# Performance work log

Measured on AMD Instinct MI355X. Metric: run time of the kernel, lower is better.

The kernel has to match this reference:

```python
import jax, jax.numpy as jnp
import numpy as np

NE, NT, NC, D, NR = 100000, 1024, 128, 128, 500
H, E, L_GCN = 8, 4, 2
B, DEG = 512, 8
NSRC = B * DEG
NNZ_E2T, NNZ_T2C, NNZ_E2C = 1000000, 50000, 500000
TAU, DECAY, CLW = 0.5, 1e-4, 0.1
N_NODES = NE + NT + NC


def setup_inputs() -> dict:
    ks = iter(jax.random.split(jax.random.key(0), 64))
    def n(shape, s=0.05):
        return jax.random.normal(next(ks), shape, jnp.float32) * s
    def ri(shape, hi):
        return jax.random.randint(next(ks), shape, 0, hi, jnp.int32)
    def u(shape):
        return jax.random.uniform(next(ks), shape, jnp.float32) * 0.01
    T = NT
    return {
        'entity_emb': n((NE, D)), 'type_emb': n((NT, D)), 'cluster_emb': n((NC, D)),
        'relation': n((NR, 2 * D)),
        'ln_g': jnp.ones((D,), jnp.float32), 'ln_b': jnp.zeros((D,), jnp.float32),
        'cl_w1': n((D, D)), 'cl_b1': jnp.zeros((D,), jnp.float32),
        'cl_w2': n((D, D)), 'cl_b2': jnp.zeros((D,), jnp.float32),
        'fc_w': n((2 * D, T)), 'fc_b': jnp.zeros((T,), jnp.float32),
        'wq': n((T, T)), 'bq': jnp.zeros((T,), jnp.float32),
        'wk': n((T, T)), 'bk': jnp.zeros((T,), jnp.float32),
        'wv': n((T, T)), 'bv': jnp.zeros((T,), jnp.float32),
        'wo': n((T, T)), 'bo': jnp.zeros((T,), jnp.float32),
        'gate_w': n((T, E)), 'exp_w': n((E, T, T)), 'exp_b': jnp.zeros((E, T), jnp.float32),
        'e2t_val': u((NNZ_E2T,)), 't2c_val': u((NNZ_T2C,)), 'e2c_val': u((NNZ_E2C,)),
        'e2t_row': ri((NNZ_E2T,), NE + NT), 'e2t_col': ri((NNZ_E2T,), NE + NT),
        't2c_row': ri((NNZ_T2C,), NT + NC), 't2c_col': ri((NNZ_T2C,), NT + NC),
        'e2c_row': ri((NNZ_E2C,), NE + NC), 'e2c_col': ri((NNZ_E2C,), NE + NC),
        'src_ids': ri((NSRC,), N_NODES), 'etype': ri((NSRC,), 2 * NR),
    }


def _light_gcn(ea, eb, row, col, val, na, nb):
    x = jnp.concatenate([ea, eb], axis=0)
    acc = x
    for _ in range(L_GCN):  # fixed small layer count
        x = jax.ops.segment_sum(val[:, None] * x[col], row, num_segments=na + nb)
        acc = acc + x
    m = acc / (L_GCN + 1)
    return m[:na], m[na:]


def _ln(x, g, b):
    mu = x.mean(-1, keepdims=True)
    var = x.var(-1, keepdims=True)
    return (x - mu) * jax.lax.rsqrt(var + 1e-5) * g + b


def _cl_loss(src1, src2, w1, b1, w2, b2):
    def proj(x):
        return jax.nn.elu(x @ w1 + b1) @ w2 + b2
    def norm(x):
        return x / jnp.maximum(jnp.linalg.norm(x, axis=1, keepdims=True), 1e-12)
    z1, z2 = norm(proj(src1)), norm(proj(src2))
    s11 = jnp.exp(z1 @ z1.T / TAU)   # [N,N]
    s12 = jnp.exp(z1 @ z2.T / TAU)
    s22 = jnp.exp(z2 @ z2.T / TAU)
    d12 = jnp.diag(s12)
    l1 = -jnp.log(d12 / (s11.sum(1) + s12.sum(1) - jnp.diag(s11)))
    l2 = -jnp.log(d12 / (s22.sum(1) + s12.sum(0) - jnp.diag(s22)))
    return ((l1 + l2) * 0.5).mean()


def _mha_moe(x, wq, bq, wk, bk, wv, bv, wo, bo, gate_w, exp_w, exp_b):
    # x: [B, DEG, T]; MHA over mailbox axis, then softmax-gated MoE, mean-pool.
    b, l, t = x.shape
    dh = t // H
    q = (x @ wq + bq).reshape(b, l, H, dh)
    k = (x @ wk + bk).reshape(b, l, H, dh)
    v = (x @ wv + bv).reshape(b, l, H, dh)
    attn = jax.nn.softmax(jnp.einsum('blhd,bmhd->bhlm', q, k) / jnp.sqrt(jnp.float32(dh)), axis=-1)
    o = jnp.einsum('bhlm,bmhd->blhd', attn, v).reshape(b, l, t) @ wo + bo
    gate = jax.nn.softmax(o @ gate_w, axis=-1)               # [B,L,E]
    eo = jnp.einsum('blt,etu->bleu', o, exp_w) + exp_b       # [B,L,E,T]
    moe = jnp.einsum('ble,blet->blt', gate, eo)
    return moe.mean(axis=1)                                  # [B,T]


def reference(entity_emb, type_emb, cluster_emb, relation, ln_g, ln_b,
              cl_w1, cl_b1, cl_w2, cl_b2, fc_w, fc_b,
              wq, bq, wk, bk, wv, bv, wo, bo, gate_w, exp_w, exp_b,
              e2t_val, t2c_val, e2c_val,
              e2t_row, e2t_col, t2c_row, t2c_col, e2c_row, e2c_col,
              src_ids, etype):
    e2t_e, e2t_t = _light_gcn(entity_emb, type_emb, e2t_row, e2t_col, e2t_val, NE, NT)
    t2c_t, t2c_c = _light_gcn(type_emb, cluster_emb, t2c_row, t2c_col, t2c_val, NT, NC)
    e2c_e, e2c_c = _light_gcn(entity_emb, cluster_emb, e2c_row, e2c_col, e2c_val, NE, NC)
    # with_norm=True path; dropout is eval-mode identity
    e2t_e, e2t_t = _ln(e2t_e, ln_g, ln_b), _ln(e2t_t, ln_g, ln_b)
    t2c_t, t2c_c = _ln(t2c_t, ln_g, ln_b), _ln(t2c_c, ln_g, ln_b)
    e2c_e, e2c_c = _ln(e2c_e, ln_g, ln_b), _ln(e2c_c, ln_g, ln_b)
    node1 = jnp.concatenate([e2t_e, e2t_t, t2c_c], axis=0)
    node2 = jnp.concatenate([e2c_e, t2c_t, e2c_c], axis=0)
    src1 = node1[src_ids]   # [NSRC, D]
    src2 = node2[src_ids]
    cl = _cl_loss(src1, src2, cl_w1, cl_b1, cl_w2, cl_b2)
    src = jnp.concatenate([src1, src2], axis=-1)  # [NSRC, 2D]
    sign = jnp.where(etype >= NR, -1.0, 1.0).astype(jnp.float32)[:, None]
    rel = relation[etype % NR] * sign
    emb_loss = DECAY * ((src ** 2).sum() + (rel ** 2).sum()) * 0.5 / rel.shape[0]
    aux_loss = CLW * cl + emb_loss
    # update_all: u_add_e message, regular mailbox [B, DEG, 2D]
    msg = jax.nn.relu(src + rel).reshape(B, DEG, 2 * D)
    predict = msg @ fc_w + fc_b                                  # [B, DEG, NT]
    predict = _mha_moe(predict, wq, bq, wk, bk, wv, bv, wo, bo, gate_w, exp_w, exp_b)
    out = jax.nn.sigmoid(predict)                                # [B, NT]
    return out, aux_loss
```

## Files before the change

kernel.cpp:

```cpp
#include <hip/hip_runtime.h>
#include <hip/hip_bf16.h>
#include <cmath>

constexpr int cNE = 100000, cNT = 1024, cNC = 128, cD = 128, cNR = 500;
constexpr int cB = 512, cNSRC = 4096, cT = 1024, cE = 4;
constexpr int cNNZ_E2T = 1000000, cNNZ_T2C = 50000, cNNZ_E2C = 500000;
constexpr float cDECAY = 1e-4f, cCLW = 0.1f;
constexpr int cNN_E2T = cNE + cNT;
constexpr int cNN_E2C = cNE + cNC;
constexpr int cNN_T2C = cNT + cNC;

constexpr size_t F_S1   = 0;
constexpr size_t F_S2   = F_S1 + 524288;
constexpr size_t F_PT   = F_S2 + 524288;
constexpr size_t F_Z1   = F_PT + 524288;
constexpr size_t F_Z2   = F_Z1 + 524288;
constexpr size_t F_MSG  = F_Z2 + 524288;
constexpr size_t F_GATE = F_MSG + 524288;
constexpr size_t F_SCAL = F_GATE + 16384;
constexpr size_t F_RS   = F_SCAL + 64;
constexpr size_t F_D11  = F_RS + 16384;
constexpr size_t F_D12  = F_D11 + 4096;
constexpr size_t F_D22  = F_D12 + 4096;
constexpr size_t F_U    = F_D22 + 4096;
constexpr size_t G_X1F  = F_U;
constexpr size_t G_X2C  = G_X1F + 6465536;
constexpr size_t G_SLOT = G_X2C + 262144;
constexpr size_t G_REP  = G_SLOT + 101376;
constexpr size_t G_RP   = G_REP + 4096;
constexpr size_t G_FILL = G_RP + 101376;
constexpr size_t G_COLS = G_FILL + 101376;
constexpr size_t G_VALS = G_COLS + 1000000;
constexpr size_t G_X1T  = G_VALS + 1000000;
constexpr size_t G_X2T  = G_X1T + 73728;
constexpr size_t G_BSUM = G_X2T + 73728;
constexpr size_t A_U0  = F_U;
constexpr size_t A_U1  = F_U + 2097152;
constexpr size_t A_WBT = F_U + 4 * 2097152;

typedef __attribute__((ext_vector_type(8))) short short8v;
typedef __attribute__((ext_vector_type(4))) float f32x4;

__device__ __forceinline__ void atomAdd(float* p, float v) {
  __hip_atomic_fetch_add(p, v, __ATOMIC_RELAXED, __HIP_MEMORY_SCOPE_AGENT);
}
__device__ __forceinline__ ushort f2bf(float f) {
  __hip_bfloat16 h = __float2bfloat16(f);
  return *reinterpret_cast<ushort*>(&h);
}
__device__ __forceinline__ float bf2f(ushort u) {
  __hip_bfloat16 h; *reinterpret_cast<ushort*>(&h) = u;
  return __bfloat162float(h);
}

__device__ __forceinline__ int mapNode(int mode, int id) {
  switch (mode) {
    case 0:  return (id < cNE + cNT) ? id : -1;
    case 1:  return (id >= cNE + cNT) ? (id - cNE) : -1;
    case 2:  return (id >= cNE && id < cNE + cNT) ? (id - cNE) : -1;
    default: return (id < cNE) ? id
                   : ((id >= cNE + cNT) ? (id - cNT) : -1);
  }
}

__device__ __forceinline__ float blockReduce256(float v, float* sh, int tid) {
  sh[tid] = v; __syncthreads();
  for (int s = 128; s > 0; s >>= 1) {
    if (tid < s) sh[tid] += sh[tid + s];
    __syncthreads();
  }
  float r = sh[0]; __syncthreads();
  return r;
}

__global__ __launch_bounds__(256) void k_init3(int* __restrict__ slot, int* __restrict__ mark,
                                               int* __restrict__ fill, int n) {
  int i = blockIdx.x * 256 + threadIdx.x;
  if (i < n) { slot[i] = 0x7f7f7f7f; mark[i] = 0; fill[i] = 0; }
}

__global__ __launch_bounds__(256) void k_slot_mark(const int* __restrict__ ids,
                                                   int* __restrict__ slot,
                                                   int* __restrict__ mark, int mode) {
  int i = blockIdx.x * 256 + threadIdx.x;
  if (i >= cNSRC) return;
  int node = mapNode(mode, ids[i]);
  if (node >= 0) { atomicMin(&slot[node], i); mark[node] = 1; }
}

__global__ __launch_bounds__(256) void k_mark_edges(const int* __restrict__ row,
                                                    const int* __restrict__ col, int nnz,
                                                    const int* __restrict__ slot,
                                                    int* __restrict__ mark) {
  int e = blockIdx.x * 256 + threadIdx.x;
  if (e >= nnz) return;
  int r = row[e];
  if (slot[r] < cNSRC) mark[col[e]] = 1;
}

__global__ __launch_bounds__(256) void k_hist(const int* __restrict__ row, int nnz,
                                              const int* __restrict__ mark,
                                              int* __restrict__ cnt) {
  int e = blockIdx.x * 256 + threadIdx.x;
  if (e >= nnz) return;
  int r = row[e];
// ... 32 lines not shown
  }
  if (tid < nb) bsum[tid] = sh[tid] - v;
  if (tid == 511) rowptr[n] = sh[511];
}

__global__ __launch_bounds__(256) void k_scan_add(int* __restrict__ rowptr,
                                                  const int* __restrict__ bsum, int n,
                                                  int* __restrict__ fill) {
  int i = blockIdx.x * 256 + threadIdx.x;
  if (i < n) {
    int r = rowptr[i] + bsum[blockIdx.x];
    rowptr[i] = r;
    fill[i] = r;
  }
}

__global__ __launch_bounds__(256) void k_fill(const int* __restrict__ row,
                                              const int* __restrict__ col,
                                              const float* __restrict__ val, int nnz,
                                              const int* __restrict__ mark,
                                              int* __restrict__ fill,
                                              int* __restrict__ cols, float* __restrict__ vals) {
  int e = blockIdx.x * 256 + threadIdx.x;
  if (e >= nnz) return;
  int r = row[e];
  if (mark && !mark[r]) return;
  int pos = atomicAdd(&fill[r], 1);
  cols[pos] = col[e];
  vals[pos] = val[e];
}

__global__ __launch_bounds__(256) void k_gather(
    const int* __restrict__ rowptr, const int* __restrict__ cols, const float* __restrict__ vals,
    const float* __restrict__ ea, const float* __restrict__ eb, int na,
    int nrows, const int* __restrict__ mark, ushort* __restrict__ out) {
  int r = blockIdx.x * 4 + (threadIdx.x >> 6);
  if (r >= nrows) return;
  if (mark && !mark[r]) return;
  int lane = threadIdx.x & 63;
  int p0 = rowptr[r], p1 = rowptr[r + 1];
  float ax = 0.f, ay = 0.f;
  int p = p0;
  for (; p + 2 <= p1; p += 2) {
    int c0 = cols[p], c1 = cols[p + 1];
    float v0 = vals[p], v1 = vals[p + 1];
    const float* s0 = (c0 < na) ? (ea + (size_t)c0 * cD) : (eb + (size_t)(c0 - na) * cD);
    const float* s1 = (c1 < na) ? (ea + (size_t)c1 * cD) : (eb + (size_t)(c1 - na) * cD);
    float2 x0 = *reinterpret_cast<const float2*>(s0 + lane * 2);
    float2 x1 = *reinterpret_cast<const float2*>(s1 + lane * 2);
    ax += v0 * x0.x + v1 * x1.x;
    ay += v0 * x0.y + v1 * x1.y;
  }
  if (p < p1) {
    int c = cols[p];
    float v = vals[p];
    const float* s = (c < na) ? (ea + (size_t)c * cD) : (eb + (size_t)(c - na) * cD);
    float2 x = *reinterpret_cast<const float2*>(s + lane * 2);
    ax += v * x.x; ay += v * x.y;
  }
  ushort2 o; o.x = f2bf(ax); o.y = f2bf(ay);
  *reinterpret_cast<ushort2*>(out + (size_t)r * cD + lane * 2) = o;
}

__global__ __launch_bounds__(256) void k_rep(const int* __restrict__ ids,
                                             const int* __restrict__ slot, int mode,
                                             int* __restrict__ rep) {
  int i = blockIdx.x * 256 + threadIdx.x;
  if (i >= cNSRC) return;
  int node = mapNode(mode, ids[i]);
  rep[i] = (node >= 0 && slot[node] == i) ? node : -1;
}

__global__ __launch_bounds__(256) void k_gather_slot(
    const int* __restrict__ rowptr, const int* __restrict__ cols, const float* __restrict__ vals,
    const ushort* __restrict__ x1, const int* __restrict__ rep,
    ushort* __restrict__ outc) {
  int i = blockIdx.x * 4 + (threadIdx.x >> 6);
  if (i >= cNSRC) return;
  int r = rep[i];
  if (r < 0) return;
  int lane = threadIdx.x & 63;
  int p0 = rowptr[r], p1 = rowptr[r + 1];
  float ax = 0.f, ay = 0.f;
  int p = p0;
  for (; p + 2 <= p1; p += 2) {
    int c0 = cols[p], c1 = cols[p + 1];
    float v0 = vals[p], v1 = vals[p + 1];
    ushort2 x0 = *reinterpret_cast<const ushort2*>(x1 + (size_t)c0 * cD + lane * 2);
    ushort2 x1v = *reinterpret_cast<const ushort2*>(x1 + (size_t)c1 * cD + lane * 2);
    ax += v0 * bf2f(x0.x) + v1 * bf2f(x1v.x);
    ay += v0 * bf2f(x0.y) + v1 * bf2f(x1v.y);
  }
  if (p < p1) {
    int c = cols[p];
    float v = vals[p];
    ushort2 x = *reinterpret_cast<const ushort2*>(x1 + (size_t)c * cD + lane * 2);
    ax += v * bf2f(x.x); ay += v * bf2f(x.y);
  }
  ushort2 o; o.x = f2bf(ax); o.y = f2bf(ay);
  *reinterpret_cast<ushort2*>(outc + (size_t)i * cD + lane * 2) = o;
}

__global__ __launch_bounds__(256) void k_gather_bf(
    const int* __restrict__ rowptr, const int* __restrict__ cols, const float* __restrict__ vals,
    const ushort* __restrict__ x1, int nrows, ushort* __restrict__ out) {
  int r = blockIdx.x * 4 + (threadIdx.x >> 6);
  if (r >= nrows) return;
  int lane = threadIdx.x & 63;
  int p0 = rowptr[r], p1 = rowptr[r + 1];
  float ax = 0.f, ay = 0.f;
  for (int p = p0; p < p1; ++p) {
    int c = cols[p];
    float v = vals[p];
    ushort2 x = *reinterpret_cast<const ushort2*>(x1 + (size_t)c * cD + lane * 2);
    ax += v * bf2f(x.x); ay += v * bf2f(x.y);
  }
  ushort2 o; o.x = f2bf(ax); o.y = f2bf(ay);
  *reinterpret_cast<ushort2*>(out + (size_t)r * cD + lane * 2) = o;
}

__global__ __launch_bounds__(128) void gather_ln(
    const int* __restrict__ ids, int mode,
    const float* __restrict__ ea, const float* __restrict__ eb, int na,
    const ushort* __restrict__ x1, const ushort* __restrict__ x2, const int* __restrict__ slot,
    const float* __restrict__ g, const float* __restrict__ bia, float* __restrict__ dst) {
  __shared__ float shx[2], shy[2];
// ... 178 lines not shown
      short8v af[2], bfr[2];
#pragma unroll
      for (int i = 0; i < 2; ++i)
        af[i] = *reinterpret_cast<const short8v*>(&As[(wr + i * 16 + la) * 40 + lk]);
#pragma unroll
      for (int j = 0; j < 2; ++j)
        bfr[j] = *reinterpret_cast<const short8v*>(&Bs[(wc + j * 16 + la) * 40 + lk]);
#pragma unroll
      for (int i = 0; i < 2; ++i)
#pragma unroll
        for (int j = 0; j < 2; ++j)
          acc[i][j] = __builtin_amdgcn_mfma_f32_16x16x32_bf16(af[i], bfr[j], acc[i][j], 0, 0, 0);
    }
  }
  const int r0 = by * 64 + wr + (lane >> 4) * 4;
  const int c0 = bx * 64 + wc + la;
#pragma unroll
  for (int i = 0; i < 2; ++i)
#pragma unroll
    for (int q = 0; q < 4; ++q) {
      int r = r0 + i * 16 + q;
      float4 gv = *reinterpret_cast<const float4*>(gsum + r * 4);
#pragma unroll
      for (int j = 0; j < 2; ++j) {
        int c = c0 + j * 16;
        float bias = gv.x * expb[c] + gv.y * expb[1024 + c] +
                     gv.z * expb[2048 + c] + gv.w * expb[3072 + c];
        float s = (acc[i][j][q] + bias) * 0.125f;
        out[(size_t)r * 1024 + c] = 1.0f / (1.0f + expf(-s));
      }
    }
}

__global__ __launch_bounds__(256) void gram_sym(
    const ushort* __restrict__ W, float* __restrict__ rsum,
    float* __restrict__ d11, float* __restrict__ d12, float* __restrict__ d22) {
  __shared__ ushort As[128 * 40];
  __shared__ ushort Bs[128 * 40];
  int tt = blockIdx.x, bi = 0, cnt = 64;
  while (tt >= cnt) { tt -= cnt; ++bi; --cnt; }
  int bj = bi + tt;
  const bool diag = (bi == bj);
  const int t = threadIdx.x;
  const int wv = t >> 6, lane = t & 63;
  const int wr = (wv >> 1) * 64, wc = (wv & 1) * 64;
  const int srow = t >> 1, shalf = t & 1;
  const ushort* Ag = W + (size_t)(bi * 128 + srow) * 128 + shalf * 16;
  const ushort* Bg = W + (size_t)(bj * 128 + srow) * 128 + shalf * 16;
  uint4 ra0 = *reinterpret_cast<const uint4*>(Ag);
  uint4 ra1 = *reinterpret_cast<const uint4*>(Ag + 8);
  uint4 rb0 = *reinterpret_cast<const uint4*>(Bg);
  uint4 rb1 = *reinterpret_cast<const uint4*>(Bg + 8);
  f32x4 acc[4][4];
  const f32x4 z4 = {0.f, 0.f, 0.f, 0.f};
#pragma unroll
  for (int i = 0; i < 4; ++i)
#pragma unroll
    for (int j = 0; j < 4; ++j) acc[i][j] = z4;
  const int la = lane & 15, lk = (lane >> 4) * 8;
  const int sdst = srow * 40 + shalf * 16;
  for (int kt = 0; kt < 128; kt += 32) {
    __syncthreads();
    *reinterpret_cast<uint4*>(&As[sdst])     = ra0;
    *reinterpret_cast<uint4*>(&As[sdst + 8]) = ra1;
    *reinterpret_cast<uint4*>(&Bs[sdst])     = rb0;
    *reinterpret_cast<uint4*>(&Bs[sdst + 8]) = rb1;
    __syncthreads();
    if (kt + 32 < 128) {
      ra0 = *reinterpret_cast<const uint4*>(Ag + kt + 32);
      ra1 = *reinterpret_cast<const uint4*>(Ag + kt + 40);
      rb0 = *reinterpret_cast<const uint4*>(Bg + kt + 32);
      rb1 = *reinterpret_cast<const uint4*>(Bg + kt + 40);
    }
    short8v af[4], bfr[4];
#pragma unroll
    for (int i = 0; i < 4; ++i)
      af[i] = *reinterpret_cast<const short8v*>(&As[(wr + i * 16 + la) * 40 + lk]);
#pragma unroll
    for (int j = 0; j < 4; ++j)
      bfr[j] = *reinterpret_cast<const short8v*>(&Bs[(wc + j * 16 + la) * 40 + lk]);
#pragma unroll
    for (int i = 0; i < 4; ++i)
#pragma unroll
      for (int j = 0; j < 4; ++j)
        acc[i][j] = __builtin_amdgcn_mfma_f32_16x16x32_bf16(af[i], bfr[j], acc[i][j], 0, 0, 0);
  }
  const int r0 = bi * 128 + wr + (lane >> 4) * 4;
  const int c0 = bj * 128 + wc + la;
  constexpr float K2 = 2.8853900817779268f;
  float rs[4][4];
  float cs[4] = {0.f, 0.f, 0.f, 0.f};
#pragma unroll
  for (int i = 0; i < 4; ++i)
#pragma unroll
    for (int q = 0; q < 4; ++q) rs[i][q] = 0.f;
#pragma unroll
  for (int i = 0; i < 4; ++i)
#pragma unroll
    for (int j = 0; j < 4; ++j)
#pragma unroll
      for (int q = 0; q < 4; ++q) {
        int r = r0 + i * 16 + q;
        int c = c0 + j * 16;
        float e = exp2f(K2 * acc[i][j][q]);
        rs[i][q] += e;
        cs[j] += e;
        if (c == r)        { if (r < 4096) d11[r] = e; else d22[r - 4096] = e; }
        if (c == r + 4096) d12[r] = e;
      }
#pragma unroll
  for (int m = 1; m < 16; m <<= 1)
#pragma unroll
    for (int i = 0; i < 4; ++i)
#pragma unroll
      for (int q = 0; q < 4; ++q) rs[i][q] += __shfl_xor(rs[i][q], m);
  float* rowdst = rsum + ((bj >= 32) ? 8192 : 0);
  if (la == 0) {
#pragma unroll
    for (int i = 0; i < 4; ++i)
#pragma unroll
      for (int q = 0; q < 4; ++q) atomAdd(&rowdst[r0 + i * 16 + q], rs[i][q]);
  }
  if (!diag) {
#pragma unroll
    for (int j = 0; j < 4; ++j) {
      cs[j] += __shfl_xor(cs[j], 16);
      cs[j] += __shfl_xor(cs[j], 32);
    }
    float* coldst = rsum + ((bi >= 32) ? 8192 : 0);
    if ((lane >> 4) == 0) {
#pragma unroll
      for (int j = 0; j < 4; ++j) atomAdd(&coldst[c0 + j * 16], cs[j]);
    }
  }
}

__global__ __launch_bounds__(256) void cl_row(
    const float* __restrict__ rsum, const float* __restrict__ d11,
    const float* __restrict__ d12, const float* __restrict__ d22,
    float* __restrict__ cl_sum) {
  __shared__ float sh[256];
  int i = blockIdx.x * 256 + threadIdx.x;
  float denA = rsum[i] + rsum[8192 + i] - d11[i];
  float denB = rsum[8192 + 4096 + i] + rsum[4096 + i] - d22[i];
  float l = 0.5f * (logf(denA) + logf(denB)) - logf(d12[i]);
  float s = blockReduce256(l, sh, threadIdx.x);
  if (threadIdx.x == 0) atomAdd(cl_sum, s);
}

__global__ __launch_bounds__(256) void k_wt_bt(const float* __restrict__ W,
                                               ushort* __restrict__ Bt, int K, int N) {
  __shared__ float tile[32][33];
  int n0 = blockIdx.x * 32, k0 = blockIdx.y * 32;
  int tx = threadIdx.x & 31, ty = threadIdx.x >> 5;
#pragma unroll
  for (int i = 0; i < 4; ++i)
    tile[ty + 8 * i][tx] = W[(size_t)(k0 + ty + 8 * i) * N + n0 + tx];
  __syncthreads();
#pragma unroll
  for (int i = 0; i < 4; ++i)
    Bt[(size_t)(n0 + ty + 8 * i) * K + k0 + tx] = f2bf(tile[tx][ty + 8 * i]);
}

__global__ __launch_bounds__(256) void k_wt_bt_s(const float* __restrict__ Wbase,
                                                 ushort* __restrict__ Btbase, int K, int N) {
// ... 152 lines not shown
  const int* t2c_row = (const int*)d_in[28];
  const int* t2c_col = (const int*)d_in[29];
  const int* e2c_row = (const int*)d_in[30];
  const int* e2c_col = (const int*)d_in[31];
  const int* src_ids = (const int*)d_in[32];
  const int* etype   = (const int*)d_in[33];

  float* ws = (float*)d_ws;
  float* S1 = ws + F_S1;
  float* S2 = ws + F_S2;
  ushort* Wbf = (ushort*)(ws + F_PT);
  ushort* P1bf = (ushort*)(ws + F_Z1);
  ushort* SBbf = (ushort*)(ws + F_Z2);
  ushort* MSGbf = (ushort*)(ws + F_MSG);
  float* GSUM = ws + F_GATE;
  float* SCAL = ws + F_SCAL;
  float* RS   = ws + F_RS;
  float* BQKV = ws + F_RS;
  float* D11  = ws + F_D11;
  float* D12  = ws + F_D12;
  float* D22  = ws + F_D22;
  ushort* X1F = (ushort*)(ws + G_X1F);
  ushort* X2C = (ushort*)(ws + G_X2C);
  int*   MARK = (int*)(ws + G_X2C);
  int*   SLOT = (int*)(ws + G_SLOT);
  int*   REP  = (int*)(ws + G_REP);
  int*   RP   = (int*)(ws + G_RP);
  int*   FILL = (int*)(ws + G_FILL);
  int*   COLS = (int*)(ws + G_COLS);
  float* VALS = ws + G_VALS;
  ushort* X1T = (ushort*)(ws + G_X1T);
  ushort* X2T = (ushort*)(ws + G_X2T);
  int*   BSUM = (int*)(ws + G_BSUM);
  ushort* PB   = (ushort*)(ws + A_U0);
  ushort* AE   = (ushort*)(ws + A_U0);
  ushort* QKV  = (ushort*)(ws + A_U1);
  ushort* OB   = (ushort*)(ws + A_U1);
  ushort* WBT  = (ushort*)(ws + A_WBT);

  hipMemsetAsync(SCAL, 0, 2 * sizeof(float), stream);
  hipMemsetAsync(RS, 0, (16384 + 3 * 4096) * sizeof(float), stream);

  auto run_gcn_masked = [&](const int* row, const int* col, const float* val, int nnz, int nn,
                            const float* ea, const float* eb, int na, int mode,
                            float* dst) {
    int nb = (nn + 255) / 256;
    int gEdge = (nnz + 255) / 256;
    k_init3<<<nb, 256, 0, stream>>>(SLOT, MARK, FILL, nn);
    k_slot_mark<<<16, 256, 0, stream>>>(src_ids, SLOT, MARK, mode);
    k_mark_edges<<<gEdge, 256, 0, stream>>>(row, col, nnz, SLOT, MARK);
    k_hist<<<gEdge, 256, 0, stream>>>(row, nnz, MARK, FILL);
    k_scan_block<<<nb, 256, 0, stream>>>(FILL, nn, RP, BSUM);
    k_bsum_scan<<<1, 512, 0, stream>>>(BSUM, nb, RP, nn);
    k_scan_add<<<nb, 256, 0, stream>>>(RP, BSUM, nn, FILL);
    k_fill<<<gEdge, 256, 0, stream>>>(row, col, val, nnz, MARK, FILL, COLS, VALS);
    k_rep<<<16, 256, 0, stream>>>(src_ids, SLOT, mode, REP);
    k_gather<<<(nn + 3) / 4, 256, 0, stream>>>(RP, COLS, VALS, ea, eb, na, nn, MARK, X1F);
    k_gather_slot<<<cNSRC / 4, 256, 0, stream>>>(RP, COLS, VALS, X1F, REP, X2C);
    gather_ln<<<cNSRC, 128, 0, stream>>>(src_ids, mode, ea, eb, na, X1F, X2C, SLOT,
                                         ln_g, ln_b, dst);
  };

  run_gcn_masked(e2t_row, e2t_col, e2t_val, cNNZ_E2T, cNN_E2T, entity, type_e, cNE, 0, S1);
  run_gcn_masked(e2c_row, e2c_col, e2c_val, cNNZ_E2C, cNN_E2C, entity, cluster, cNE, 3, S2);

  {
    int nn = cNN_T2C, nb = (nn + 255) / 256, gEdge = (cNNZ_T2C + 255) / 256;
    hipMemsetAsync(FILL, 0, (size_t)nn * sizeof(int), stream);
    k_hist<<<gEdge, 256, 0, stream>>>(t2c_row, cNNZ_T2C, nullptr, FILL);
    k_scan_block<<<nb, 256, 0, stream>>>(FILL, nn, RP, BSUM);
    k_bsum_scan<<<1, 512, 0, stream>>>(BSUM, nb, RP, nn);
    k_scan_add<<<nb, 256, 0, stream>>>(RP, BSUM, nn, FILL);
    k_fill<<<gEdge, 256, 0, stream>>>(t2c_row, t2c_col, t2c_val, cNNZ_T2C, nullptr,
                                      FILL, COLS, VALS);
    k_gather<<<(nn + 3) / 4, 256, 0, stream>>>(RP, COLS, VALS, type_e, cluster, cNT,
                                               nn, nullptr, X1T);
    k_gather_bf<<<(nn + 3) / 4, 256, 0, stream>>>(RP, COLS, VALS, X1T, nn, X2T);
    gather_ln<<<cNSRC, 128, 0, stream>>>(src_ids, 1, type_e, cluster, cNT, X1T, X2T, nullptr,
                                         ln_g, ln_b, S1);
    gather_ln<<<cNSRC, 128, 0, stream>>>(src_ids, 2, type_e, cluster, cNT, X1T, X2T, nullptr,
                                         ln_g, ln_b, S2);
  }

  k_post_s<<<128, 256, 0, stream>>>(S1, S2, relation, etype, SBbf, MSGbf, SCAL + 1);

  ushort* W1T = WBT;
  ushort* W2T = WBT + 16384;
  k_wt_bt<<<dim3(4, 4), 256, 0, stream>>>(cl_w1, W1T, cD, cD);
  k_wt_bt<<<dim3(4, 4), 256, 0, stream>>>(cl_w2, W2T, cD, cD);
  gemm_bf<<<dim3(1, 64), 256, 0, stream>>>(SBbf, W1T, cD, cD, cl_b1, P1bf, 1);
  gemm_bf<<<dim3(1, 64), 256, 0, stream>>>(P1bf, W2T, cD, cD, cl_b2, Wbf, 0);
  rownorm_bf2<<<2 * cNSRC, 128, 0, stream>>>(Wbf);
  gram_sym<<<2080, 256, 0, stream>>>(Wbf, RS, D11, D12, D22);
  cl_row<<<16, 256, 0, stream>>>(RS, D11, D12, D22, SCAL);

  k_wt_bt<<<dim3(cT / 32, 256 / 32), 256, 0, stream>>>(fc_w, WBT, 256, cT);
  gemm_bf<<<dim3(cT / 128, cNSRC / 128), 256, 0, stream>>>(MSGbf, WBT, cT, 256, fc_b, PB, 0);

  k_wt_bt3<<<dim3(32, 32, 3), 256, 0, stream>>>(wq, wk, wv, WBT, cT, cT);
  hipMemcpyAsync(BQKV,        bq, cT * sizeof(float), hipMemcpyDeviceToDevice, stream);
  hipMemcpyAsync(BQKV + 1024, bk, cT * sizeof(float), hipMemcpyDeviceToDevice, stream);
  hipMemcpyAsync(BQKV + 2048, bv, cT * sizeof(float), hipMemcpyDeviceToDevice, stream);
  gemm_bf<<<dim3(3072 / 128, cNSRC / 128), 256, 0, stream>>>(PB, WBT, 3072, cT, BQKV, QKV, 0);
  mha_attn<<<cB * 8, 64, 0, stream>>>(QKV, PB);
  k_wt_bt<<<dim3(32, 32), 256, 0, stream>>>(wo, WBT, cT, cT);
  gemm_bf<<<dim3(cT / 128, cNSRC / 128), 256, 0, stream>>>(PB, WBT, cT, cT, bo, OB, 0);

  k_gate_pool<<<cB, 256, 0, stream>>>(OB, gate_w, AE, GSUM);
  k_wt_bt_s<<<dim3(32, 32, 4), 256, 0, stream>>>(exp_w, WBT, cT, cT);
  gemm_moe2<<<dim3(16, 8), 256, 0, stream>>>(AE, WBT, exp_b, GSUM, (float*)d_out);

  finalize_k<<<1, 1, 0, stream>>>(SCAL, (float*)d_out + (size_t)cB * cT);
}
```

Measured before the change: 535.4 us.

## Gather GCN features from bf16 copies and strip-tile the contrastive Gram kernel

Converts the entity, type and cluster embedding tables to bf16 once, so the sparse GCN first-layer gathers read half as many bytes per neighbor row. The symmetric Gram/exp kernel is also restructured: each block now keeps its A row-tile resident in shared memory across up to four B column tiles, with register prefetch of the next B tile. This cuts launched blocks from 2080 to 544 and reduces redundant A loads and row-sum atomics. The cost is an extra conversion pass over the 100k-row entity table each call, slightly lower precision in the gathered sums, and larger shared memory per block, which may lower occupancy.

```diff
diff --git a/kernel.cpp b/kernel.cpp
--- a/kernel.cpp
+++ b/kernel.cpp
@@ -34,6 +34,9 @@
 constexpr size_t G_X1T  = G_VALS + 1000000;
 constexpr size_t G_X2T  = G_X1T + 73728;
 constexpr size_t G_BSUM = G_X2T + 73728;
+constexpr size_t G_EBF  = G_BSUM + 512;
+constexpr size_t G_TBF  = G_EBF + 3200000;
+constexpr size_t G_CBF  = G_TBF + 65536;
 constexpr size_t A_U0  = F_U;
 constexpr size_t A_U1  = F_U + 2097152;
 constexpr size_t A_WBT = F_U + 4 * 2097152;
@@ -71,6 +74,16 @@
   }
   float r = sh[0]; __syncthreads();
   return r;
+}
+
+__global__ __launch_bounds__(256) void k_to_bf(const float* __restrict__ src,
+                                               ushort* __restrict__ dst, int nq) {
+  for (int q = blockIdx.x * 256 + threadIdx.x; q < nq; q += gridDim.x * 256) {
+    float4 v = *reinterpret_cast<const float4*>(src + (size_t)q * 4);
+    ushort4 o;
+    o.x = f2bf(v.x); o.y = f2bf(v.y); o.z = f2bf(v.z); o.w = f2bf(v.w);
+    *reinterpret_cast<ushort4*>(dst + (size_t)q * 4) = o;
+  }
 }
 
 __global__ __launch_bounds__(256) void k_init3(int* __restrict__ slot, int* __restrict__ mark,
@@ -169,7 +182,7 @@
 
 __global__ __launch_bounds__(256) void k_gather(
     const int* __restrict__ rowptr, const int* __restrict__ cols, const float* __restrict__ vals,
-    const float* __restrict__ ea, const float* __restrict__ eb, int na,
+    const ushort* __restrict__ ea, const ushort* __restrict__ eb, int na,
     int nrows, const int* __restrict__ mark, ushort* __restrict__ out) {
   int r = blockIdx.x * 4 + (threadIdx.x >> 6);
   if (r >= nrows) return;
@@ -181,19 +194,19 @@
   for (; p + 2 <= p1; p += 2) {
     int c0 = cols[p], c1 = cols[p + 1];
     float v0 = vals[p], v1 = vals[p + 1];
-    const float* s0 = (c0 < na) ? (ea + (size_t)c0 * cD) : (eb + (size_t)(c0 - na) * cD);
-    const float* s1 = (c1 < na) ? (ea + (size_t)c1 * cD) : (eb + (size_t)(c1 - na) * cD);
-    float2 x0 = *reinterpret_cast<const float2*>(s0 + lane * 2);
-    float2 x1 = *reinterpret_cast<const float2*>(s1 + lane * 2);
-    ax += v0 * x0.x + v1 * x1.x;
-    ay += v0 * x0.y + v1 * x1.y;
+    const ushort* s0 = (c0 < na) ? (ea + (size_t)c0 * cD) : (eb + (size_t)(c0 - na) * cD);
+    const ushort* s1 = (c1 < na) ? (ea + (size_t)c1 * cD) : (eb + (size_t)(c1 - na) * cD);
+    ushort2 x0 = *reinterpret_cast<const ushort2*>(s0 + lane * 2);
+    ushort2 x1 = *reinterpret_cast<const ushort2*>(s1 + lane * 2);
+    ax += v0 * bf2f(x0.x) + v1 * bf2f(x1.x);
+    ay += v0 * bf2f(x0.y) + v1 * bf2f(x1.y);
   }
   if (p < p1) {
     int c = cols[p];
     float v = vals[p];
-    const float* s = (c < na) ? (ea + (size_t)c * cD) : (eb + (size_t)(c - na) * cD);
-    float2 x = *reinterpret_cast<const float2*>(s + lane * 2);
-    ax += v * x.x; ay += v * x.y;
+    const ushort* s = (c < na) ? (ea + (size_t)c * cD) : (eb + (size_t)(c - na) * cD);
+    ushort2 x = *reinterpret_cast<const ushort2*>(s + lane * 2);
+    ax += v * bf2f(x.x); ay += v * bf2f(x.y);
   }
   ushort2 o; o.x = f2bf(ax); o.y = f2bf(ay);
   *reinterpret_cast<ushort2*>(out + (size_t)r * cD + lane * 2) = o;
@@ -473,105 +486,156 @@
     }
 }
 
-__global__ __launch_bounds__(256) void gram_sym(
+__global__ __launch_bounds__(256) void gram_strip(
     const ushort* __restrict__ W, float* __restrict__ rsum,
     float* __restrict__ d11, float* __restrict__ d12, float* __restrict__ d22) {
-  __shared__ ushort As[128 * 40];
-  __shared__ ushort Bs[128 * 40];
-  int tt = blockIdx.x, bi = 0, cnt = 64;
-  while (tt >= cnt) { tt -= cnt; ++bi; --cnt; }
-  int bj = bi + tt;
-  const bool diag = (bi == bj);
+  __shared__ ushort As[4 * 128 * 40];
+  __shared__ ushort Bs[4 * 128 * 40];
+  int rem = blockIdx.x, bi = 0;
+  for (;;) { int ch = (64 - bi + 3) >> 2; if (rem < ch) break; rem -= ch; ++bi; }
+  const int bj0 = bi + (rem << 2);
+  const int bjend = (bj0 + 4 < 64) ? bj0 + 4 : 64;
   const int t = threadIdx.x;
   const int wv = t >> 6, lane = t & 63;
   const int wr = (wv >> 1) * 64, wc = (wv & 1) * 64;
   const int srow = t >> 1, shalf = t & 1;
-  const ushort* Ag = W + (size_t)(bi * 128 + srow) * 128 + shalf * 16;
-  const ushort* Bg = W + (size_t)(bj * 128 + srow) * 128 + shalf * 16;
-  uint4 ra0 = *reinterpret_cast<const uint4*>(Ag);
-  uint4 ra1 = *reinterpret_cast<const uint4*>(Ag + 8);
-  uint4 rb0 = *reinterpret_cast<const uint4*>(Bg);
-  uint4 rb1 = *reinterpret_cast<const uint4*>(Bg + 8);
-  f32x4 acc[4][4];
-  const f32x4 z4 = {0.f, 0.f, 0.f, 0.f};
+  const int la = lane & 15, lk = (lane >> 4) * 8;
+  const int soff = srow * 40 + shalf * 16;
+  constexpr float K2 = 2.8853900817779268f;
+
+  {
+    const ushort* Ag = W + (size_t)(bi * 128 + srow) * 128 + shalf * 16;
+#pragma unroll
+    for (int kc = 0; kc < 4; ++kc) {
+      uint4 a0 = *reinterpret_cast<const uint4*>(Ag + kc * 32);
+      uint4 a1 = *reinterpret_cast<const uint4*>(Ag + kc * 32 + 8);
+      *reinterpret_cast<uint4*>(&As[kc * 5120 + soff])     = a0;
+      *reinterpret_cast<uint4*>(&As[kc * 5120 + soff + 8]) = a1;
+    }
+  }
+  uint4 rb[8];
+  {
+    const ushort* Bg = W + (size_t)(bj0 * 128 + srow) * 128 + shalf * 16;
+#pragma unroll
+    for (int kc = 0; kc < 4; ++kc) {
+      rb[2 * kc]     = *reinterpret_cast<const uint4*>(Bg + kc * 32);
+      rb[2 * kc + 1] = *reinterpret_cast<const uint4*>(Bg + kc * 32 + 8);
+    }
+  }
+  float rsLo[4][4], rsHi[4][4];
 #pragma unroll
   for (int i = 0; i < 4; ++i)
 #pragma unroll
-    for (int j = 0; j < 4; ++j) acc[i][j] = z4;
-  const int la = lane & 15, lk = (lane >> 4) * 8;
-  const int sdst = srow * 40 + shalf * 16;
-  for (int kt = 0; kt < 128; kt += 32) {
+    for (int q = 0; q < 4; ++q) { rsLo[i][q] = 0.f; rsHi[i][q] = 0.f; }
+  const int r0 = bi * 128 + wr + (lane >> 4) * 4;
+
+  for (int bj = bj0; bj < bjend; ++bj) {
     __syncthreads();
-    *reinterpret_cast<uint4*>(&As[sdst])     = ra0;
-    *reinterpret_cast<uint4*>(&As[sdst + 8]) = ra1;
-    *reinterpret_cast<uint4*>(&Bs[sdst])     = rb0;
-    *reinterpret_cast<uint4*>(&Bs[sdst + 8]) = rb1;
+#pragma unroll
+    for (int kc = 0; kc < 4; ++kc) {
+      *reinterpret_cast<uint4*>(&Bs[kc * 5120 + soff])     = rb[2 * kc];
+      *reinterpret_cast<uint4*>(&Bs[kc * 5120 + soff + 8]) = rb[2 * kc + 1];
+    }
     __syncthreads();
-    if (kt + 32 < 128) {
-      ra0 = *reinterpret_cast<const uint4*>(Ag + kt + 32);
-      ra1 = *reinterpret_cast<const uint4*>(Ag + kt + 40);
-      rb0 = *reinterpret_cast<const uint4*>(Bg + kt + 32);
-      rb1 = *reinterpret_cast<const uint4*>(Bg + kt + 40);
-    }
-    short8v af[4], bfr[4];
+    if (bj + 1 < bjend) {
+      const ushort* Bg = W + (size_t)((bj + 1) * 128 + srow) * 128 + shalf * 16;
+#pragma unroll
+      for (int kc = 0; kc < 4; ++kc) {
+        rb[2 * kc]     = *reinterpret_cast<const uint4*>(Bg + kc * 32);
+        rb[2 * kc + 1] = *reinterpret_cast<const uint4*>(Bg + kc * 32 + 8);
+      }
+    }
+    f32x4 acc[4][4];
+    const f32x4 z4 = {0.f, 0.f, 0.f, 0.f};
 #pragma unroll
     for (int i = 0; i < 4; ++i)
-      af[i] = *reinterpret_cast<const short8v*>(&As[(wr + i * 16 + la) * 40 + lk]);
-#pragma unroll
-    for (int j = 0; j < 4; ++j)
-      bfr[j] = *reinterpret_cast<const short8v*>(&Bs[(wc + j * 16 + la) * 40 + lk]);
+#pragma unroll
+      for (int j = 0; j < 4; ++j) acc[i][j] = z4;
+#pragma unroll
+    for (int kc = 0; kc < 4; ++kc) {
+      short8v af[4], bfr[4];
+#pragma unroll
+      for (int i = 0; i < 4; ++i)
+        af[i] = *reinterpret_cast<const short8v*>(&As[kc * 5120 + (wr + i * 16 + la) * 40 + lk]);
+#pragma unroll
+      for (int j = 0; j < 4; ++j)
+        bfr[j] = *reinterpret_cast<const short8v*>(&Bs[kc * 5120 + (wc + j * 16 + la) * 40 + lk]);
+#pragma unroll
+      for (int i = 0; i < 4; ++i)
+#pragma unroll
+        for (int j = 0; j < 4; ++j)
+          acc[i][j] = __builtin_amdgcn_mfma_f32_16x16x32_bf16(af[i], bfr[j], acc[i][j], 0, 0, 0);
+    }
+    const int c0 = bj * 128 + wc + la;
+    const bool isDiag = (bj == bi);
+    const bool isD12  = (bj == bi + 32);
+    float cs4[4] = {0.f, 0.f, 0.f, 0.f};
+    if (bj >= 32) {
+#pragma unroll
+      for (int i = 0; i < 4; ++i)
+#pragma unroll
+        for (int j = 0; j < 4; ++j)
+#pragma unroll
+          for (int q = 0; q < 4; ++q) {
+            int r = r0 + i * 16 + q;
+            int c = c0 + j * 16;
+            float e = exp2f(K2 * acc[i][j][q]);
+            rsHi[i][q] += e;
+            cs4[j] += e;
+            if (isDiag && c == r) { if (r < 4096) d11[r] = e; else d22[r - 4096] = e; }
+            if (isD12 && c == r + 4096) d12[r] = e;
+          }
+    } else {
+#pragma unroll
+      for (int i = 0; i < 4; ++i)
+#pragma unroll
+        for (int j = 0; j < 4; ++j)
+#pragma unroll
+          for (int q = 0; q < 4; ++q) {
+            int r = r0 + i * 16 + q;
+            int c = c0 + j * 16;
+            float e = exp2f(K2 * acc[i][j][q]);
+            rsLo[i][q] += e;
+            cs4[j] += e;
+            if (isDiag && c == r) { if (r < 4096) d11[r] = e; else d22[r - 4096] = e; }
+          }
+    }
+    if (!isDiag) {
+#pragma unroll
+      for (int j = 0; j < 4; ++j) {
+        cs4[j] += __shfl_xor(cs4[j], 16);
+        cs4[j] += __shfl_xor(cs4[j], 32);
+      }
+      float* coldst = rsum + ((bi >= 32) ? 8192 : 0);
+      if ((lane >> 4) == 0) {
+#pragma unroll
+        for (int j = 0; j < 4; ++j) atomAdd(&coldst[c0 + j * 16], cs4[j]);
+      }
+    }
+  }
+  const bool hasLo = (bj0 < 32);
+  const bool hasHi = (bjend > 32);
+#pragma unroll
+  for (int m = 1; m < 16; m <<= 1)
 #pragma unroll
     for (int i = 0; i < 4; ++i)
 #pragma unroll
-      for (int j = 0; j < 4; ++j)
-        acc[i][j] = __builtin_amdgcn_mfma_f32_16x16x32_bf16(af[i], bfr[j], acc[i][j], 0, 0, 0);
-  }
-  const int r0 = bi * 128 + wr + (lane >> 4) * 4;
-  const int c0 = bj * 128 + wc + la;
-  constexpr float K2 = 2.8853900817779268f;
-  float rs[4][4];
-  float cs[4] = {0.f, 0.f, 0.f, 0.f};
-#pragma unroll
-  for (int i = 0; i < 4; ++i)
-#pragma unroll
-    for (int q = 0; q < 4; ++q) rs[i][q] = 0.f;
-#pragma unroll
-  for (int i = 0; i < 4; ++i)
-#pragma unroll
-    for (int j = 0; j < 4; ++j)
-#pragma unroll
       for (int q = 0; q < 4; ++q) {
-        int r = r0 + i * 16 + q;
-        int c = c0 + j * 16;
-        float e = exp2f(K2 * acc[i][j][q]);
-        rs[i][q] += e;
-        cs[j] += e;
-        if (c == r)        { if (r < 4096) d11[r] = e; else d22[r - 4096] = e; }
-        if (c == r + 4096) d12[r] = e;
+        rsLo[i][q] += __shfl_xor(rsLo[i][q], m);
+        rsHi[i][q] += __shfl_xor(rsHi[i][q], m);
       }
-#pragma unroll
-  for (int m = 1; m < 16; m <<= 1)
-#pragma unroll
-    for (int i = 0; i < 4; ++i)
-#pragma unroll
-      for (int q = 0; q < 4; ++q) rs[i][q] += __shfl_xor(rs[i][q], m);
-  float* rowdst = rsum + ((bj >= 32) ? 8192 : 0);
   if (la == 0) {
-#pragma unroll
-    for (int i = 0; i < 4; ++i)
-#pragma unroll
-      for (int q = 0; q < 4; ++q) atomAdd(&rowdst[r0 + i * 16 + q], rs[i][q]);
-  }
-  if (!diag) {
-#pragma unroll
-    for (int j = 0; j < 4; ++j) {
-      cs[j] += __shfl_xor(cs[j], 16);
-      cs[j] += __shfl_xor(cs[j], 32);
-    }
-    float* coldst = rsum + ((bi >= 32) ? 8192 : 0);
-    if ((lane >> 4) == 0) {
-#pragma unroll
-      for (int j = 0; j < 4; ++j) atomAdd(&coldst[c0 + j * 16], cs[j]);
+    if (hasLo) {
+#pragma unroll
+      for (int i = 0; i < 4; ++i)
+#pragma unroll
+        for (int q = 0; q < 4; ++q) atomAdd(&rsum[r0 + i * 16 + q], rsLo[i][q]);
+    }
+    if (hasHi) {
+#pragma unroll
+      for (int i = 0; i < 4; ++i)
+#pragma unroll
+        for (int q = 0; q < 4; ++q) atomAdd(&rsum[8192 + r0 + i * 16 + q], rsHi[i][q]);
     }
   }
 }
@@ -790,6 +854,9 @@
   ushort* X1T = (ushort*)(ws + G_X1T);
   ushort* X2T = (ushort*)(ws + G_X2T);
   int*   BSUM = (int*)(ws + G_BSUM);
+  ushort* EBF = (ushort*)(ws + G_EBF);
+  ushort* TBF = (ushort*)(ws + G_TBF);
+  ushort* CBF = (ushort*)(ws + G_CBF);
   ushort* PB   = (ushort*)(ws + A_U0);
   ushort* AE   = (ushort*)(ws + A_U0);
   ushort* QKV  = (ushort*)(ws + A_U1);
@@ -799,8 +866,13 @@
   hipMemsetAsync(SCAL, 0, 2 * sizeof(float), stream);
   hipMemsetAsync(RS, 0, (16384 + 3 * 4096) * sizeof(float), stream);
 
+  k_to_bf<<<2048, 256, 0, stream>>>(entity, EBF, cNE * cD / 4);
+  k_to_bf<<<128, 256, 0, stream>>>(type_e, TBF, cNT * cD / 4);
+  k_to_bf<<<16, 256, 0, stream>>>(cluster, CBF, cNC * cD / 4);
+
   auto run_gcn_masked = [&](const int* row, const int* col, const float* val, int nnz, int nn,
-                            const float* ea, const float* eb, int na, int mode,
+                            const float* ea_f, const float* eb_f,
+                            const ushort* ea_b, const ushort* eb_b, int na, int mode,
                             float* dst) {
     int nb = (nn + 255) / 256;
     int gEdge = (nnz + 255) / 256;
@@ -813,14 +885,16 @@
     k_scan_add<<<nb, 256, 0, stream>>>(RP, BSUM, nn, FILL);
     k_fill<<<gEdge, 256, 0, stream>>>(row, col, val, nnz, MARK, FILL, COLS, VALS);
     k_rep<<<16, 256, 0, stream>>>(src_ids, SLOT, mode, REP);
-    k_gather<<<(nn + 3) / 4, 256, 0, stream>>>(RP, COLS, VALS, ea, eb, na, nn, MARK, X1F);
+    k_gather<<<(nn + 3) / 4, 256, 0, stream>>>(RP, COLS, VALS, ea_b, eb_b, na, nn, MARK, X1F);
     k_gather_slot<<<cNSRC / 4, 256, 0, stream>>>(RP, COLS, VALS, X1F, REP, X2C);
-    gather_ln<<<cNSRC, 128, 0, stream>>>(src_ids, mode, ea, eb, na, X1F, X2C, SLOT,
+    gather_ln<<<cNSRC, 128, 0, stream>>>(src_ids, mode, ea_f, eb_f, na, X1F, X2C, SLOT,
                                          ln_g, ln_b, dst);
   };
 
-  run_gcn_masked(e2t_row, e2t_col, e2t_val, cNNZ_E2T, cNN_E2T, entity, type_e, cNE, 0, S1);
-  run_gcn_masked(e2c_row, e2c_col, e2c_val, cNNZ_E2C, cNN_E2C, entity, cluster, cNE, 3, S2);
+  run_gcn_masked(e2t_row, e2t_col, e2t_val, cNNZ_E2T, cNN_E2T,
+                 entity, type_e, EBF, TBF, cNE, 0, S1);
+  run_gcn_masked(e2c_row, e2c_col, e2c_val, cNNZ_E2C, cNN_E2C,
+                 entity, cluster, EBF, CBF, cNE, 3, S2);
 
   {
     int nn = cNN_T2C, nb = (nn + 255) / 256, gEdge = (cNNZ_T2C + 255) / 256;
@@ -831,7 +905,7 @@
     k_scan_add<<<nb, 256, 0, stream>>>(RP, BSUM, nn, FILL);
     k_fill<<<gEdge, 256, 0, stream>>>(t2c_row, t2c_col, t2c_val, cNNZ_T2C, nullptr,
                                       FILL, COLS, VALS);
-    k_gather<<<(nn + 3) / 4, 256, 0, stream>>>(RP, COLS, VALS, type_e, cluster, cNT,
+    k_gather<<<(nn + 3) / 4, 256, 0, stream>>>(RP, COLS, VALS, TBF, CBF, cNT,
                                                nn, nullptr, X1T);
     k_gather_bf<<<(nn + 3) / 4, 256, 0, stream>>>(RP, COLS, VALS, X1T, nn, X2T);
     gather_ln<<<cNSRC, 128, 0, stream>>>(src_ids, 1, type_e, cluster, cNT, X1T, X2T, nullptr,
@@ -849,7 +923,7 @@
   gemm_bf<<<dim3(1, 64), 256, 0, stream>>>(SBbf, W1T, cD, cD, cl_b1, P1bf, 1);
   gemm_bf<<<dim3(1, 64), 256, 0, stream>>>(P1bf, W2T, cD, cD, cl_b2, Wbf, 0);
   rownorm_bf2<<<2 * cNSRC, 128, 0, stream>>>(Wbf);
-  gram_sym<<<2080, 256, 0, stream>>>(Wbf, RS, D11, D12, D22);
+  gram_strip<<<544, 256, 0, stream>>>(Wbf, RS, D11, D12, D22);
   cl_row<<<16, 256, 0, stream>>>(RS, D11, D12, D22, SCAL);
 
   k_wt_bt<<<dim3(cT / 32, 256 / 32), 256, 0, stream>>>(fc_w, WBT, 256, cT);
```

Result: slower. 567.4 us (+6.0%).

## Gather GCN features from bf16 copies of embedding tables and pack QKV biases

Applied to the files above, without the earlier changes.

Converts the entity, type and cluster embedding tables to bf16 once per call and has the first-layer sparse gathers read those bf16 copies instead of fp32. This halves the bytes fetched per random row in the gathers. The cost is a full conversion pass over the 100k x 128 entity table and a loss of precision in first-layer inputs. Gather loops are also unrolled from 2 to 4 edges, and three device memcpys for the QKV biases are replaced by a single small packing kernel.

```diff
diff --git a/kernel.cpp b/kernel.cpp
--- a/kernel.cpp
+++ b/kernel.cpp
@@ -34,6 +34,9 @@
 constexpr size_t G_X1T  = G_VALS + 1000000;
 constexpr size_t G_X2T  = G_X1T + 73728;
 constexpr size_t G_BSUM = G_X2T + 73728;
+constexpr size_t G_EBF  = G_BSUM + 512;
+constexpr size_t G_TBF  = G_EBF + 3200000;
+constexpr size_t G_CBF  = G_TBF + 65536;
 constexpr size_t A_U0  = F_U;
 constexpr size_t A_U1  = F_U + 2097152;
 constexpr size_t A_WBT = F_U + 4 * 2097152;
@@ -71,6 +74,25 @@
   }
   float r = sh[0]; __syncthreads();
   return r;
+}
+
+__global__ __launch_bounds__(256) void k_to_bf(const float* __restrict__ src,
+                                               ushort* __restrict__ dst, int nq) {
+  for (int q = blockIdx.x * 256 + threadIdx.x; q < nq; q += gridDim.x * 256) {
+    float4 v = *reinterpret_cast<const float4*>(src + (size_t)q * 4);
+    ushort4 o;
+    o.x = f2bf(v.x); o.y = f2bf(v.y); o.z = f2bf(v.z); o.w = f2bf(v.w);
+    *reinterpret_cast<ushort4*>(dst + (size_t)q * 4) = o;
+  }
+}
+
+__global__ __launch_bounds__(256) void k_pack_bias(const float* __restrict__ b0,
+                                                   const float* __restrict__ b1,
+                                                   const float* __restrict__ b2,
+                                                   float* __restrict__ dst) {
+  int i = blockIdx.x * 256 + threadIdx.x;
+  float v = (i < 1024) ? b0[i] : (i < 2048) ? b1[i - 1024] : b2[i - 2048];
+  dst[i] = v;
 }
 
 __global__ __launch_bounds__(256) void k_init3(int* __restrict__ slot, int* __restrict__ mark,
@@ -169,7 +191,7 @@
 
 __global__ __launch_bounds__(256) void k_gather(
     const int* __restrict__ rowptr, const int* __restrict__ cols, const float* __restrict__ vals,
-    const float* __restrict__ ea, const float* __restrict__ eb, int na,
+    const ushort* __restrict__ ea, const ushort* __restrict__ eb, int na,
     int nrows, const int* __restrict__ mark, ushort* __restrict__ out) {
   int r = blockIdx.x * 4 + (threadIdx.x >> 6);
   if (r >= nrows) return;
@@ -178,22 +200,26 @@
   int p0 = rowptr[r], p1 = rowptr[r + 1];
   float ax = 0.f, ay = 0.f;
   int p = p0;
-  for (; p + 2 <= p1; p += 2) {
-    int c0 = cols[p], c1 = cols[p + 1];
-    float v0 = vals[p], v1 = vals[p + 1];
-    const float* s0 = (c0 < na) ? (ea + (size_t)c0 * cD) : (eb + (size_t)(c0 - na) * cD);
-    const float* s1 = (c1 < na) ? (ea + (size_t)c1 * cD) : (eb + (size_t)(c1 - na) * cD);
-    float2 x0 = *reinterpret_cast<const float2*>(s0 + lane * 2);
-    float2 x1 = *reinterpret_cast<const float2*>(s1 + lane * 2);
-    ax += v0 * x0.x + v1 * x1.x;
-    ay += v0 * x0.y + v1 * x1.y;
-  }
-  if (p < p1) {
+  for (; p + 4 <= p1; p += 4) {
+    int c0 = cols[p], c1 = cols[p + 1], c2 = cols[p + 2], c3 = cols[p + 3];
+    float v0 = vals[p], v1 = vals[p + 1], v2 = vals[p + 2], v3 = vals[p + 3];
+    const ushort* s0 = (c0 < na) ? (ea + (size_t)c0 * cD) : (eb + (size_t)(c0 - na) * cD);
+    const ushort* s1 = (c1 < na) ? (ea + (size_t)c1 * cD) : (eb + (size_t)(c1 - na) * cD);
+    const ushort* s2 = (c2 < na) ? (ea + (size_t)c2 * cD) : (eb + (size_t)(c2 - na) * cD);
+    const ushort* s3 = (c3 < na) ? (ea + (size_t)c3 * cD) : (eb + (size_t)(c3 - na) * cD);
+    ushort2 x0 = *reinterpret_cast<const ushort2*>(s0 + lane * 2);
+    ushort2 x1 = *reinterpret_cast<const ushort2*>(s1 + lane * 2);
+    ushort2 x2 = *reinterpret_cast<const ushort2*>(s2 + lane * 2);
+    ushort2 x3 = *reinterpret_cast<const ushort2*>(s3 + lane * 2);
+    ax += v0 * bf2f(x0.x) + v1 * bf2f(x1.x) + v2 * bf2f(x2.x) + v3 * bf2f(x3.x);
+    ay += v0 * bf2f(x0.y) + v1 * bf2f(x1.y) + v2 * bf2f(x2.y) + v3 * bf2f(x3.y);
+  }
+  for (; p < p1; ++p) {
     int c = cols[p];
     float v = vals[p];
-    const float* s = (c < na) ? (ea + (size_t)c * cD) : (eb + (size_t)(c - na) * cD);
-    float2 x = *reinterpret_cast<const float2*>(s + lane * 2);
-    ax += v * x.x; ay += v * x.y;
+    const ushort* s = (c < na) ? (ea + (size_t)c * cD) : (eb + (size_t)(c - na) * cD);
+    ushort2 x = *reinterpret_cast<const ushort2*>(s + lane * 2);
+    ax += v * bf2f(x.x); ay += v * bf2f(x.y);
   }
   ushort2 o; o.x = f2bf(ax); o.y = f2bf(ay);
   *reinterpret_cast<ushort2*>(out + (size_t)r * cD + lane * 2) = o;
@@ -220,15 +246,17 @@
   int p0 = rowptr[r], p1 = rowptr[r + 1];
   float ax = 0.f, ay = 0.f;
   int p = p0;
-  for (; p + 2 <= p1; p += 2) {
-    int c0 = cols[p], c1 = cols[p + 1];
-    float v0 = vals[p], v1 = vals[p + 1];
+  for (; p + 4 <= p1; p += 4) {
+    int c0 = cols[p], c1 = cols[p + 1], c2 = cols[p + 2], c3 = cols[p + 3];
+    float v0 = vals[p], v1 = vals[p + 1], v2 = vals[p + 2], v3 = vals[p + 3];
     ushort2 x0 = *reinterpret_cast<const ushort2*>(x1 + (size_t)c0 * cD + lane * 2);
     ushort2 x1v = *reinterpret_cast<const ushort2*>(x1 + (size_t)c1 * cD + lane * 2);
-    ax += v0 * bf2f(x0.x) + v1 * bf2f(x1v.x);
-    ay += v0 * bf2f(x0.y) + v1 * bf2f(x1v.y);
-  }
-  if (p < p1) {
+    ushort2 x2 = *reinterpret_cast<const ushort2*>(x1 + (size_t)c2 * cD + lane * 2);
+    ushort2 x3 = *reinterpret_cast<const ushort2*>(x1 + (size_t)c3 * cD + lane * 2);
+    ax += v0 * bf2f(x0.x) + v1 * bf2f(x1v.x) + v2 * bf2f(x2.x) + v3 * bf2f(x3.x);
+    ay += v0 * bf2f(x0.y) + v1 * bf2f(x1v.y) + v2 * bf2f(x2.y) + v3 * bf2f(x3.y);
+  }
+  for (; p < p1; ++p) {
     int c = cols[p];
     float v = vals[p];
     ushort2 x = *reinterpret_cast<const ushort2*>(x1 + (size_t)c * cD + lane * 2);
@@ -790,6 +818,9 @@
   ushort* X1T = (ushort*)(ws + G_X1T);
   ushort* X2T = (ushort*)(ws + G_X2T);
   int*   BSUM = (int*)(ws + G_BSUM);
+  ushort* EBF = (ushort*)(ws + G_EBF);
+  ushort* TBF = (ushort*)(ws + G_TBF);
+  ushort* CBF = (ushort*)(ws + G_CBF);
   ushort* PB   = (ushort*)(ws + A_U0);
   ushort* AE   = (ushort*)(ws + A_U0);
   ushort* QKV  = (ushort*)(ws + A_U1);
@@ -799,8 +830,13 @@
   hipMemsetAsync(SCAL, 0, 2 * sizeof(float), stream);
   hipMemsetAsync(RS, 0, (16384 + 3 * 4096) * sizeof(float), stream);
 
+  k_to_bf<<<2048, 256, 0, stream>>>(entity, EBF, cNE * cD / 4);
+  k_to_bf<<<128, 256, 0, stream>>>(type_e, TBF, cNT * cD / 4);
+  k_to_bf<<<16, 256, 0, stream>>>(cluster, CBF, cNC * cD / 4);
+
   auto run_gcn_masked = [&](const int* row, const int* col, const float* val, int nnz, int nn,
-                            const float* ea, const float* eb, int na, int mode,
+                            const float* ea_f, const float* eb_f,
+                            const ushort* ea_b, const ushort* eb_b, int na, int mode,
                             float* dst) {
     int nb = (nn + 255) / 256;
     int gEdge = (nnz + 255) / 256;
@@ -813,14 +849,16 @@
     k_scan_add<<<nb, 256, 0, stream>>>(RP, BSUM, nn, FILL);
     k_fill<<<gEdge, 256, 0, stream>>>(row, col, val, nnz, MARK, FILL, COLS, VALS);
     k_rep<<<16, 256, 0, stream>>>(src_ids, SLOT, mode, REP);
-    k_gather<<<(nn + 3) / 4, 256, 0, stream>>>(RP, COLS, VALS, ea, eb, na, nn, MARK, X1F);
+    k_gather<<<(nn + 3) / 4, 256, 0, stream>>>(RP, COLS, VALS, ea_b, eb_b, na, nn, MARK, X1F);
     k_gather_slot<<<cNSRC / 4, 256, 0, stream>>>(RP, COLS, VALS, X1F, REP, X2C);
-    gather_ln<<<cNSRC, 128, 0, stream>>>(src_ids, mode, ea, eb, na, X1F, X2C, SLOT,
+    gather_ln<<<cNSRC, 128, 0, stream>>>(src_ids, mode, ea_f, eb_f, na, X1F, X2C, SLOT,
                                          ln_g, ln_b, dst);
   };
 
-  run_gcn_masked(e2t_row, e2t_col, e2t_val, cNNZ_E2T, cNN_E2T, entity, type_e, cNE, 0, S1);
-  run_gcn_masked(e2c_row, e2c_col, e2c_val, cNNZ_E2C, cNN_E2C, entity, cluster, cNE, 3, S2);
+  run_gcn_masked(e2t_row, e2t_col, e2t_val, cNNZ_E2T, cNN_E2T,
+                 entity, type_e, EBF, TBF, cNE, 0, S1);
+  run_gcn_masked(e2c_row, e2c_col, e2c_val, cNNZ_E2C, cNN_E2C,
+                 entity, cluster, EBF, CBF, cNE, 3, S2);
 
   {
     int nn = cNN_T2C, nb = (nn + 255) / 256, gEdge = (cNNZ_T2C + 255) / 256;
@@ -831,7 +869,7 @@
     k_scan_add<<<nb, 256, 0, stream>>>(RP, BSUM, nn, FILL);
     k_fill<<<gEdge, 256, 0, stream>>>(t2c_row, t2c_col, t2c_val, cNNZ_T2C, nullptr,
                                       FILL, COLS, VALS);
-    k_gather<<<(nn + 3) / 4, 256, 0, stream>>>(RP, COLS, VALS, type_e, cluster, cNT,
+    k_gather<<<(nn + 3) / 4, 256, 0, stream>>>(RP, COLS, VALS, TBF, CBF, cNT,
                                                nn, nullptr, X1T);
     k_gather_bf<<<(nn + 3) / 4, 256, 0, stream>>>(RP, COLS, VALS, X1T, nn, X2T);
     gather_ln<<<cNSRC, 128, 0, stream>>>(src_ids, 1, type_e, cluster, cNT, X1T, X2T, nullptr,
@@ -856,9 +894,7 @@
   gemm_bf<<<dim3(cT / 128, cNSRC / 128), 256, 0, stream>>>(MSGbf, WBT, cT, 256, fc_b, PB, 0);
 
   k_wt_bt3<<<dim3(32, 32, 3), 256, 0, stream>>>(wq, wk, wv, WBT, cT, cT);
-  hipMemcpyAsync(BQKV,        bq, cT * sizeof(float), hipMemcpyDeviceToDevice, stream);
-  hipMemcpyAsync(BQKV + 1024, bk, cT * sizeof(float), hipMemcpyDeviceToDevice, stream);
-  hipMemcpyAsync(BQKV + 2048, bv, cT * sizeof(float), hipMemcpyDeviceToDevice, stream);
+  k_pack_bias<<<12, 256, 0, stream>>>(bq, bk, bv, BQKV);
   gemm_bf<<<dim3(3072 / 128, cNSRC / 128), 256, 0, stream>>>(PB, WBT, 3072, cT, BQKV, QKV, 0);
   mha_attn<<<cB * 8, 64, 0, stream>>>(QKV, PB);
   k_wt_bt<<<dim3(32, 32), 256, 0, stream>>>(wo, WBT, cT, cT);
```

Measured after the change: 529.5 us. No clear change (-1.1%).
